# Performance work log

Hardware: AMD Instinct MI355X
Metric: run time of the kernel (lower is better)

The kernel has to match this reference:

```python
import jax, jax.numpy as jnp
import numpy as np
from jax import lax

CHUNK = 64
D_CONV = 4
EPS = 1e-5


def _rmsnorm(x, w):
    ms = jnp.mean(jnp.square(x.astype(jnp.float32)), axis=-1, keepdims=True)
    return x * lax.rsqrt(ms + EPS).astype(x.dtype) * w


def _conv_mix(x, proj_w, gate_w, conv_w, conv_b, out_proj_w):
    # x: [B,L,D] -> depthwise causal conv on projected channels, silu gate, out proj
    B, L, D = x.shape
    val = jnp.einsum('bld,ed->ble', x, proj_w)            # [B,L,d_inner]
    v = val.transpose(0, 2, 1)                            # [B,d_inner,L]
    d_inner = proj_w.shape[0]
    v = lax.conv_general_dilated(
        v, conv_w, window_strides=(1,), padding=[(D_CONV - 1, 0)],
        dimension_numbers=('NCH', 'OIH', 'NCH'), feature_group_count=d_inner)
    v = v + conv_b[None, :, None]
    val = jax.nn.silu(v.transpose(0, 2, 1))               # [B,L,d_inner]
    gate = jax.nn.silu(jnp.einsum('bld,ed->ble', x, gate_w))
    return jnp.einsum('ble,de->bld', val * gate, out_proj_w)


def _memory_attend(out, write_w, read_w, decay, log_alpha):
    B, T, D = out.shape
    C = CHUNK
    out32 = out.astype(jnp.float32)
    gamma = jax.nn.sigmoid(decay)
    log_gamma = jnp.log(gamma)
    v = jnp.einsum('btd,ed->bte', out32, write_w)         # proj_write
    wk = jnp.pad(out32[:, :-1], ((0, 0), (1, 0), (0, 0)))  # shifted keys
    rk = out32
    p = jnp.arange(C, dtype=jnp.float32)
    gp = gamma ** p                                       # [C]
    gw = gamma ** (C - 1 - p)                              # [C]
    diffs = jnp.maximum(p[:, None] - 1.0 - p[None, :], 0.0)
    M = jnp.exp(diffs * log_gamma) * (p[:, None] > p[None, :])  # [C,C]
    gC = gamma ** C
    Nc = T // C
    # scan axis first: [Nc,B,C,D]
    rk_c = rk.reshape(B, Nc, C, D).transpose(1, 0, 2, 3)
    wk_c = wk.reshape(B, Nc, C, D).transpose(1, 0, 2, 3)
    v_c = v.reshape(B, Nc, C, D).transpose(1, 0, 2, 3)

    def step(W, chunk):
        r, k, vv = chunk                                  # each [B,C,D]
        inter = jnp.einsum('bcd,bed->bce', r, W) * gp[None, :, None]
        S = jnp.einsum('bcd,bed->bce', r, k)              # [B,C,C]
        intra = jnp.einsum('bce,bed->bcd', S * M, vv)
        W_new = gC * W + jnp.einsum('bcd,bce->bde', vv * gw[None, :, None], k)
        return W_new, inter + intra

    W0 = jnp.zeros((B, D, D), dtype=jnp.float32)
    _, reads = lax.scan(step, W0, (rk_c, wk_c, v_c))      # [Nc,B,C,D]
    reads = reads.transpose(1, 0, 2, 3).reshape(B, T, D)
    read_out = jnp.einsum('btd,ed->bte', reads, read_w)
    return out + jnp.exp(log_alpha) * read_out.astype(out.dtype)


def setup_inputs() -> dict:
    key = jax.random.key(0)
    ks = jax.random.split(key, 9)
    B, T, D, d_inner = 8, 4096, 768, 1536
    s_d = 1.0 / np.sqrt(D)
    s_i = 1.0 / np.sqrt(d_inner)
    return {
        'x': jax.random.normal(ks[0], (B, T, D), jnp.float32),
        'norm_w': jnp.ones((D,), jnp.float32),
        'proj_w': jax.random.normal(ks[1], (d_inner, D), jnp.float32) * s_d,
        'gate_w': jax.random.normal(ks[2], (d_inner, D), jnp.float32) * s_d,
        'conv_w': jax.random.normal(ks[3], (d_inner, 1, D_CONV), jnp.float32) * 0.5,
        'conv_b': jnp.zeros((d_inner,), jnp.float32),
        'out_proj_w': jax.random.normal(ks[4], (D, d_inner), jnp.float32) * s_i,
        'write_w': jax.random.normal(ks[5], (D, D), jnp.float32) * s_d,
        'read_w': jax.random.normal(ks[6], (D, D), jnp.float32) * s_d,
        'decay': jnp.float32(4.6),
        'log_alpha': jnp.log(jnp.float32(0.03)),
    }


def reference(x, norm_w, proj_w, gate_w, conv_w, conv_b, out_proj_w, write_w, read_w, decay, log_alpha):
    out = _conv_mix(_rmsnorm(x, norm_w), proj_w, gate_w, conv_w, conv_b, out_proj_w)
    out = _memory_attend(out, write_w, read_w, decay, log_alpha)
    return x + out
```

## Files before the change

### kernel.cpp

```cpp
#include <hip/hip_runtime.h>
#include <stdint.h>


typedef short bf16s;
typedef __attribute__((ext_vector_type(8))) short short8;
typedef __attribute__((ext_vector_type(4))) float f32x4;

#define DEVINL __device__ __forceinline__

DEVINL float bf2f(short s) {
    union { unsigned u; float f; } v; v.u = ((unsigned)(unsigned short)s) << 16; return v.f;
}
DEVINL short f2bf(float f) {
    union { float f; unsigned u; } v; v.f = f;
    unsigned r = v.u + 0x7fffu + ((v.u >> 16) & 1u);
    return (short)(r >> 16);
}

DEVINL void glds16(void* lds, const void* g) {
    __builtin_amdgcn_global_load_lds(
        (const __attribute__((address_space(1))) void*)g,
        (__attribute__((address_space(3))) void*)lds, 16, 0, 0);
}

DEVINL void stage128(bf16s* lds, const bf16s* g, long gstride, int wave) {
#pragma unroll
    for (int p = 0; p < 4; ++p)
        glds16(lds + p * 2048 + wave * 512, g + (long)p * 32 * gstride);
}

DEVINL short8 fragr(const bf16s* t, int row, int kk, int q) {
    int f = kk * 4 + q;
    return *(const short8*)(t + row * 64 + ((f ^ (row & 7)) * 8));
}

#define MFMA(a, b, c) __builtin_amdgcn_mfma_f32_16x16x32_bf16((a), (b), (c), 0, 0, 0)

__global__ __launch_bounds__(256) void cast_w_kernel(
    const float* __restrict__ proj, const float* __restrict__ gate,
    const float* __restrict__ op, const float* __restrict__ wr, const float* __restrict__ rd,
    bf16s* __restrict__ w_pg, bf16s* __restrict__ w_op, bf16s* __restrict__ w_wr,
    bf16s* __restrict__ w_rd) {
    long i = (long)blockIdx.x * 256 + threadIdx.x;
    if (i < 1179648)        w_pg[i] = f2bf(proj[i]);
    else if (i < 2359296)   w_pg[i] = f2bf(gate[i - 1179648]);
    else if (i < 3538944)   w_op[i - 2359296] = f2bf(op[i - 2359296]);
    else if (i < 4128768)   w_wr[i - 3538944] = f2bf(wr[i - 3538944]);
    else if (i < 4718592)   w_rd[i - 4128768] = f2bf(rd[i - 4128768]);
}

__global__ __launch_bounds__(256) void rmsnorm_kernel(
    const float* __restrict__ x, const float* __restrict__ w, bf16s* __restrict__ xn) {
    long row = blockIdx.x;
    const float* xr = x + row * 768;
    int tid = threadIdx.x;
    float v0 = xr[tid], v1 = xr[tid + 256], v2 = xr[tid + 512];
    float ss = v0 * v0 + v1 * v1 + v2 * v2;
#pragma unroll
    for (int off = 32; off; off >>= 1) ss += __shfl_down(ss, off);
    __shared__ float p[4];
    if ((tid & 63) == 0) p[tid >> 6] = ss;
    __syncthreads();
    float tot = p[0] + p[1] + p[2] + p[3];
    float s = rsqrtf(tot * (1.0f / 768.0f) + 1e-5f);
    bf16s* o = xn + row * 768;
    o[tid]       = f2bf(v0 * s * w[tid]);
    o[tid + 256] = f2bf(v1 * s * w[tid + 256]);
    o[tid + 512] = f2bf(v2 * s * w[tid + 512]);
}

template <int MODE>
__global__ __launch_bounds__(256, 2) void gemm_kernel(
    const bf16s* __restrict__ A, const bf16s* __restrict__ B, int K, int N,
    bf16s* __restrict__ Cb, const float* __restrict__ xres,
    const bf16s* __restrict__ outres, const float* __restrict__ p_la,
    float* __restrict__ Cout) {
    __shared__ bf16s sA[128 * 64];
    __shared__ bf16s sB[128 * 64];
    const int tid = threadIdx.x;
    const int wave = tid >> 6, lane = tid & 63;
    const int wm = wave >> 1, wn = wave & 1;
    const int ln15 = lane & 15, q = lane >> 4;
    const long m0 = (long)blockIdx.y * 128, n0 = (long)blockIdx.x * 128;
    const int sr = tid >> 3;
    const int sf = (tid & 7) ^ (sr & 7);
    const bf16s* gA = A + (m0 + sr) * K + sf * 8;
    const bf16s* gB = B + (n0 + sr) * K + sf * 8;
    f32x4 acc[4][4] = {};
    const int nkt = K >> 6;
    for (int kt = 0; kt < nkt; ++kt) {
        __syncthreads();
        stage128(sA, gA, K, wave);
        stage128(sB, gB, K, wave);
        gA += 64; gB += 64;
        asm volatile("s_waitcnt vmcnt(0)" ::: "memory");
        __syncthreads();
#pragma unroll
        for (int kk = 0; kk < 2; ++kk) {
            short8 af[4], bf_[4];
#pragma unroll
            for (int i = 0; i < 4; ++i) af[i] = fragr(sA, wm * 64 + i * 16 + ln15, kk, q);
#pragma unroll
            for (int j = 0; j < 4; ++j) bf_[j] = fragr(sB, wn * 64 + j * 16 + ln15, kk, q);
#pragma unroll
            for (int i = 0; i < 4; ++i)
#pragma unroll
                for (int j = 0; j < 4; ++j) acc[i][j] = MFMA(af[i], bf_[j], acc[i][j]);
        }
    }
    float alpha = 0.f;
    if (MODE == 1) alpha = __expf(p_la[0]);
#pragma unroll
    for (int i = 0; i < 4; ++i)
#pragma unroll
        for (int j = 0; j < 4; ++j) {
            long mb = m0 + wm * 64 + i * 16 + q * 4;
            long nc = n0 + wn * 64 + j * 16 + ln15;
#pragma unroll
            for (int e = 0; e < 4; ++e) {
                long m = mb + e;
                float v = acc[i][j][e];
                if (MODE == 0) {
                    Cb[m * N + nc] = f2bf(v);
                } else {
                    long idx = m * 768 + nc;
                    Cout[idx] = xres[idx] + bf2f(outres[idx]) + alpha * v;
                }
            }
        }
}

__global__ __launch_bounds__(192) void conv_kernel(
    const bf16s* __restrict__ pg, const float* __restrict__ cw,
    const float* __restrict__ cb, bf16s* __restrict__ vg) {
    const int e0 = threadIdx.x * 8;
    const long l0 = (long)blockIdx.x * 16;
    float w0[8], w1[8], w2[8], w3[8], bias[8];
#pragma unroll
    for (int i = 0; i < 8; ++i) {
        const float* wc = cw + (e0 + i) * 4;
        w0[i] = wc[0]; w1[i] = wc[1]; w2[i] = wc[2]; w3[i] = wc[3];
        bias[i] = cb[e0 + i];
    }
    const bf16s* base = pg + l0 * 3072 + e0;
    short8 h0, h1, h2;
    if ((l0 & 4095) == 0) {
        short8 z = {0, 0, 0, 0, 0, 0, 0, 0};
        h0 = z; h1 = z; h2 = z;
    } else {
        h0 = *(const short8*)(base - 3 * 3072);
        h1 = *(const short8*)(base - 2 * 3072);
        h2 = *(const short8*)(base - 1 * 3072);
    }
    short8 cur = *(const short8*)base;
    short8 g8  = *(const short8*)(base + 1536);
    bf16s* out = vg + l0 * 1536 + e0;
#pragma unroll 4
    for (int t = 0; t < 16; ++t) {
        short8 ncur, ng;
        if (t < 15) {
            ncur = *(const short8*)(base + 3072);
            ng   = *(const short8*)(base + 3072 + 1536);
        }
        short8 o;
#pragma unroll
        for (int i = 0; i < 8; ++i) {
            float vv = bias[i] + bf2f(h0[i]) * w0[i] + bf2f(h1[i]) * w1[i]
                     + bf2f(h2[i]) * w2[i] + bf2f(cur[i]) * w3[i];
            float sv = vv / (1.0f + __expf(-vv));
            float gg = bf2f(g8[i]);
            o[i] = f2bf(sv * (gg / (1.0f + __expf(-gg))));
        }
        *(short8*)out = o;
        h0 = h1; h1 = h2; h2 = cur;
        cur = ncur; g8 = ng;
        base += 3072; out += 1536;
    }
}

template <int SHIFT, int GW>
__global__ __launch_bounds__(256) void transpose_kernel(
    const bf16s* __restrict__ src, bf16s* __restrict__ dst,
    const float* __restrict__ p_decay) {
    int b = blockIdx.z;
    long t0 = (long)blockIdx.y * 64, e0 = (long)blockIdx.x * 64;
    __shared__ bf16s tile[64][72];
    int tid = threadIdx.x;
    int r = tid >> 2, cs = (tid & 3) * 16;
    long tsrc = t0 + r - SHIFT;
    if (tsrc >= 0) {
        const bf16s* s = src + ((long)b * 4096 + tsrc) * 768 + e0 + cs;
        short8 v0 = *(const short8*)s;
        short8 v1 = *(const short8*)(s + 8);
        if (GW) {
            float gm = 1.0f / (1.0f + __expf(-p_decay[0]));
            float gwf = exp2f(__log2f(gm) * (float)(1023 - (int)(tsrc & 1023)));
#pragma unroll
            for (int i = 0; i < 8; ++i) {
                tile[r][cs + i]     = f2bf(bf2f(v0[i]) * gwf);
                tile[r][cs + 8 + i] = f2bf(bf2f(v1[i]) * gwf);
            }
        } else {
#pragma unroll
            for (int i = 0; i < 8; ++i) {
                tile[r][cs + i]     = v0[i];
                tile[r][cs + 8 + i] = v1[i];
            }
        }
    } else {
#pragma unroll
        for (int i = 0; i < 16; ++i) tile[r][cs + i] = 0;
    }
    __syncthreads();
    int er = tid >> 2, ts = (tid & 3) * 16;
    short8 a, bb;
#pragma unroll
    for (int i = 0; i < 8; ++i) a[i] = tile[ts + i][er];
#pragma unroll
    for (int i = 0; i < 8; ++i) bb[i] = tile[ts + 8 + i][er];
    bf16s* d = dst + ((long)b * 768 + e0 + er) * 4096 + t0 + ts;
    *(short8*)d = a;
    *(short8*)(d + 8) = bb;
}

__global__ __launch_bounds__(256, 2) void wstate_kernel(
    const bf16s* __restrict__ vTs, const bf16s* __restrict__ oTs,
    bf16s* __restrict__ Wst, const float* __restrict__ p_decay) {
    __shared__ bf16s sA[128 * 64];
    __shared__ bf16s sB[128 * 64];
    const int b = blockIdx.y;
    const int ti = blockIdx.x % 6, tj = blockIdx.x / 6;
    const int tid = threadIdx.x;
    const int wave = tid >> 6, lane = tid & 63;
    const int wm = wave >> 1, wn = wave & 1;
    const int ln15 = lane & 15, q = lane >> 4;
    const int sr = tid >> 3;
    const int sf = (tid & 7) ^ (sr & 7);
    const bf16s* gA = vTs + ((long)b * 768 + ti * 128 + sr) * 4096 + sf * 8;
    const bf16s* gB = oTs + ((long)b * 768 + tj * 128 + sr) * 4096 + sf * 8;
    const float gm = 1.0f / (1.0f + __expf(-p_decay[0]));
    const float gC = exp2f(__log2f(gm) * 1024.0f);
    f32x4 acc[4][4] = {};
    for (int jc = 0; jc < 4; ++jc) {
        bf16s* Wj = Wst + ((long)(b * 4 + jc)) * 768 * 768;
#pragma unroll
        for (int i = 0; i < 4; ++i)
#pragma unroll
            for (int jj = 0; jj < 4; ++jj) {
                long mb = ti * 128 + wm * 64 + i * 16 + q * 4;
                long nc = tj * 128 + wn * 64 + jj * 16 + ln15;
#pragma unroll
                for (int e = 0; e < 4; ++e) {
                    Wj[(mb + e) * 768 + nc] = f2bf(acc[i][jj][e]);
                    acc[i][jj][e] *= gC;
                }
            }
        for (int kt = 0; kt < 16; ++kt) {
            __syncthreads();
            stage128(sA, gA, 4096, wave);
            stage128(sB, gB, 4096, wave);
            gA += 64; gB += 64;
            asm volatile("s_waitcnt vmcnt(0)" ::: "memory");
            __syncthreads();
#pragma unroll
            for (int kk = 0; kk < 2; ++kk) {
                short8 af[4], bf_[4];
#pragma unroll
                for (int i = 0; i < 4; ++i) af[i] = fragr(sA, wm * 64 + i * 16 + ln15, kk, q);
#pragma unroll
                for (int j = 0; j < 4; ++j) bf_[j] = fragr(sB, wn * 64 + j * 16 + ln15, kk, q);
#pragma unroll
                for (int i = 0; i < 4; ++i)
#pragma unroll
                    for (int j = 0; j < 4; ++j) acc[i][j] = MFMA(af[i], bf_[j], acc[i][j]);
            }
        }
    }
}

__global__ __launch_bounds__(256, 2) void pmat_kernel(
    const bf16s* __restrict__ outb, bf16s* __restrict__ P,
    const float* __restrict__ p_decay) {
    const int ci = blockIdx.x >> 3, cj = blockIdx.x & 7;
    if (cj > ci) return;
    const int j = blockIdx.y, b = blockIdx.z;
    const bool fix = (j == 0 && cj == 0);
    __shared__ bf16s sA[128 * 64];
    __shared__ bf16s sB[128 * 64];
    const int tid = threadIdx.x;
    const int wave = tid >> 6, lane = tid & 63;
    const int wm = wave >> 1, wn = wave & 1;
    const int ln15 = lane & 15, q = lane >> 4;
    const int sr = tid >> 3;
    const int sf = (tid & 7) ^ (sr & 7);
    const bf16s* gA = outb + ((long)b * 4096 + j * 1024 + ci * 128 + sr) * 768 + sf * 8;
    const bf16s* gB = outb + ((long)b * 4096 + j * 1024 + cj * 128 + sr - 1) * 768 + sf * 8;
    f32x4 acc[4][4] = {};
    for (int kt = 0; kt < 12; ++kt) {
        __syncthreads();
        stage128(sA, gA, 768, wave);
        stage128(sB, gB, 768, wave);
        gA += 64; gB += 64;
        asm volatile("s_waitcnt vmcnt(0)" ::: "memory");
        __syncthreads();
        if (fix) {
            if (tid < 8) { short8 zz = {0,0,0,0,0,0,0,0}; ((short8*)sB)[tid] = zz; }
            __syncthreads();
        }
#pragma unroll
        for (int kk = 0; kk < 2; ++kk) {
            short8 af[4], bf_[4];
#pragma unroll
            for (int i = 0; i < 4; ++i) af[i] = fragr(sA, wm * 64 + i * 16 + ln15, kk, q);
#pragma unroll
            for (int jj = 0; jj < 4; ++jj) bf_[jj] = fragr(sB, wn * 64 + jj * 16 + ln15, kk, q);
#pragma unroll
            for (int i = 0; i < 4; ++i)
#pragma unroll
                for (int jj = 0; jj < 4; ++jj) acc[i][jj] = MFMA(af[i], bf_[jj], acc[i][jj]);
        }
    }
    const float lg = __log2f(1.0f / (1.0f + __expf(-p_decay[0])));
    bf16s* Pb = P + ((long)(b * 4 + j) << 20);
#pragma unroll
    for (int i = 0; i < 4; ++i)
#pragma unroll
        for (int jj = 0; jj < 4; ++jj) {
            int cb_ = ci * 128 + wm * 64 + i * 16 + q * 4;
            int cp  = cj * 128 + wn * 64 + jj * 16 + ln15;
#pragma unroll
            for (int e = 0; e < 4; ++e) {
                int c = cb_ + e;
                float val = (c > cp) ? acc[i][jj][e] * exp2f(lg * (float)(c - 1024)) : 0.0f;
                Pb[(long)c * 1024 + cp] = f2bf(val);
            }
        }
}

__global__ __launch_bounds__(256, 2) void reads_kernel(
    const bf16s* __restrict__ outb, const bf16s* __restrict__ Wst,
    const bf16s* __restrict__ Pm, const bf16s* __restrict__ vTs,
    bf16s* __restrict__ readsb, const float* __restrict__ p_decay) {
    const int ci = blockIdx.x & 7, vi = blockIdx.x >> 3;
    const int j = blockIdx.y, b = blockIdx.z;
    __shared__ bf16s sA[128 * 64];
    __shared__ bf16s sB[128 * 64];
    const int tid = threadIdx.x;
    const int wave = tid >> 6, lane = tid & 63;
    const int wm = wave >> 1, wn = wave & 1;
    const int ln15 = lane & 15, q = lane >> 4;
    const int sr = tid >> 3;
    const int sf = (tid & 7) ^ (sr & 7);
    const float lg = __log2f(1.0f / (1.0f + __expf(-p_decay[0])));
    f32x4 acc[4][4] = {};
    if (j > 0) {
        const bf16s* gA = outb + ((long)b * 4096 + j * 1024 + ci * 128 + sr) * 768 + sf * 8;
        const bf16s* gB = Wst + ((long)(b * 4 + j) * 768 + vi * 128 + sr) * 768 + sf * 8;
        for (int kt = 0; kt < 12; ++kt) {
            __syncthreads();
            stage128(sA, gA, 768, wave);
            stage128(sB, gB, 768, wave);
            gA += 64; gB += 64;
            asm volatile("s_waitcnt vmcnt(0)" ::: "memory");
            __syncthreads();
#pragma unroll
            for (int kk = 0; kk < 2; ++kk) {
                short8 af[4], bf_[4];
#pragma unroll
                for (int i = 0; i < 4; ++i) af[i] = fragr(sA, wm * 64 + i * 16 + ln15, kk, q);
#pragma unroll
                for (int jj = 0; jj < 4; ++jj) bf_[jj] = fragr(sB, wn * 64 + jj * 16 + ln15, kk, q);
#pragma unroll
                for (int i = 0; i < 4; ++i)
#pragma unroll
                    for (int jj = 0; jj < 4; ++jj) acc[i][jj] = MFMA(af[i], bf_[jj], acc[i][jj]);
            }
        }
#pragma unroll
        for (int i = 0; i < 4; ++i) {
            int cb_ = ci * 128 + wm * 64 + i * 16 + q * 4;
#pragma unroll
            for (int e = 0; e < 4; ++e) {
                float s = exp2f(lg * (float)(cb_ + e));
#pragma unroll
                for (int jj = 0; jj < 4; ++jj) acc[i][jj][e] *= s;
            }
        }
    }
    {
        const bf16s* gA = Pm + ((long)(b * 4 + j) << 20) + (long)(ci * 128 + sr) * 1024 + sf * 8;
        const bf16s* gB = vTs + ((long)b * 768 + vi * 128 + sr) * 4096 + j * 1024 + sf * 8;
        const int nkt = 2 * (ci + 1);
        for (int kt = 0; kt < nkt; ++kt) {
            __syncthreads();
            stage128(sA, gA, 1024, wave);
            stage128(sB, gB, 4096, wave);
            gA += 64; gB += 64;
            asm volatile("s_waitcnt vmcnt(0)" ::: "memory");
            __syncthreads();
#pragma unroll
            for (int kk = 0; kk < 2; ++kk) {
                short8 af[4], bf_[4];
#pragma unroll
                for (int i = 0; i < 4; ++i) af[i] = fragr(sA, wm * 64 + i * 16 + ln15, kk, q);
#pragma unroll
                for (int jj = 0; jj < 4; ++jj) bf_[jj] = fragr(sB, wn * 64 + jj * 16 + ln15, kk, q);
#pragma unroll
                for (int i = 0; i < 4; ++i)
#pragma unroll
                    for (int jj = 0; jj < 4; ++jj) acc[i][jj] = MFMA(af[i], bf_[jj], acc[i][jj]);
            }
        }
    }
#pragma unroll
    for (int i = 0; i < 4; ++i)
#pragma unroll
        for (int jj = 0; jj < 4; ++jj) {
            long tb = (long)j * 1024 + ci * 128 + wm * 64 + i * 16 + q * 4;
            long nc = vi * 128 + wn * 64 + jj * 16 + ln15;
#pragma unroll
            for (int e = 0; e < 4; ++e)
                readsb[((long)b * 4096 + tb + e) * 768 + nc] = f2bf(acc[i][jj][e]);
        }
}

extern "C" void kernel_launch(void* const* d_in, const int* in_sizes, int n_in,
                              void* d_out, int out_size, void* d_ws, size_t ws_size,
                              hipStream_t stream) {
    (void)in_sizes; (void)n_in; (void)out_size;
    const float* x      = (const float*)d_in[0];
    const float* norm_w = (const float*)d_in[1];
    const float* proj_w = (const float*)d_in[2];
    const float* gate_w = (const float*)d_in[3];
    const float* conv_w = (const float*)d_in[4];
    const float* conv_b = (const float*)d_in[5];
    const float* op_w   = (const float*)d_in[6];
    const float* wr_w   = (const float*)d_in[7];
    const float* rd_w   = (const float*)d_in[8];
    const float* decay  = (const float*)d_in[9];
    const float* la     = (const float*)d_in[10];

    char* ws = (char*)d_ws;
    size_t off = 0;
    auto alloc = [&](size_t bytes) { void* p = ws + off; off += (bytes + 255) & ~(size_t)255; return p; };
    bf16s* w_pg = (bf16s*)alloc(3072l * 768 * 2);
    bf16s* w_op = (bf16s*)alloc(768l * 1536 * 2);
    bf16s* w_wr = (bf16s*)alloc(768l * 768 * 2);
    bf16s* w_rd = (bf16s*)alloc(768l * 768 * 2);
    bf16s* RA   = (bf16s*)alloc(32768l * 768 * 2);
    bf16s* RB   = (bf16s*)alloc(2 * 32768l * 768 * 2);
    bf16s* RC   = (bf16s*)alloc(2 * 32768l * 768 * 2);
    bf16s* RE   = (bf16s*)alloc(32768l * 768 * 2);
    if (ws_size < off) return;

    bf16s* xn    = RA;
    bf16s* vTs   = RA;
    bf16s* pgH   = RB;
    bf16s* vb    = RB;
    bf16s* oTs   = RB + 25165824;
    bf16s* Pm    = RB;
    bf16s* vg    = RC;
    bf16s* Wst   = RC;
    bf16s* readsb= RC + 18874368;
    bf16s* outb  = RE;

    hipLaunchKernelGGL(cast_w_kernel, dim3(18432), dim3(256), 0, stream,
                       proj_w, gate_w, op_w, wr_w, rd_w, w_pg, w_op, w_wr, w_rd);
    hipLaunchKernelGGL(rmsnorm_kernel, dim3(32768), dim3(256), 0, stream, x, norm_w, xn);
    for (int h = 0; h < 2; ++h) {
        hipLaunchKernelGGL(HIP_KERNEL_NAME(gemm_kernel<0>), dim3(24, 128), dim3(256), 0, stream,
                           xn + (long)h * 16384 * 768, w_pg, 768, 3072, pgH,
                           (const float*)nullptr, (const bf16s*)nullptr, la, (float*)nullptr);
        hipLaunchKernelGGL(conv_kernel, dim3(1024), dim3(192), 0, stream,
                           pgH, conv_w, conv_b, vg + (long)h * 16384 * 1536);
    }
    hipLaunchKernelGGL(HIP_KERNEL_NAME(gemm_kernel<0>), dim3(6, 256), dim3(256), 0, stream,
                       vg, w_op, 1536, 768, outb,
                       (const float*)nullptr, (const bf16s*)nullptr, la, (float*)nullptr);
    hipLaunchKernelGGL(HIP_KERNEL_NAME(gemm_kernel<0>), dim3(6, 256), dim3(256), 0, stream,
                       outb, w_wr, 768, 768, vb,
                       (const float*)nullptr, (const bf16s*)nullptr, la, (float*)nullptr);
    hipLaunchKernelGGL(HIP_KERNEL_NAME(transpose_kernel<1, 0>), dim3(12, 64, 8), dim3(256), 0, stream,
                       outb, oTs, decay);
    hipLaunchKernelGGL(HIP_KERNEL_NAME(transpose_kernel<0, 1>), dim3(12, 64, 8), dim3(256), 0, stream,
                       vb, vTs, decay);
    hipLaunchKernelGGL(wstate_kernel, dim3(36, 8), dim3(256), 0, stream,
                       vTs, oTs, Wst, decay);
    hipLaunchKernelGGL(pmat_kernel, dim3(64, 4, 8), dim3(256), 0, stream,
                       outb, Pm, decay);
    hipLaunchKernelGGL(reads_kernel, dim3(48, 4, 8), dim3(256), 0, stream,
                       outb, Wst, Pm, vTs, readsb, decay);
    hipLaunchKernelGGL(HIP_KERNEL_NAME(gemm_kernel<1>), dim3(6, 256), dim3(256), 0, stream,
                       readsb, w_rd, 768, 768, (bf16s*)nullptr,
                       x, outb, la, (float*)d_out);
}
```

Baseline: 982.8 us.

## Replace GEMM with 256x256-tile 8-wave double-buffered pipelined kernel

Swaps the 128x128 single-buffered GEMM for a 256x256 tile kernel with 8 waves and double-buffered LDS. Global-to-LDS loads for the next k-slab are interleaved between MFMA quarters, using explicit barriers, partial vmcnt waits and setprio. This targets the load-then-compute serialization of the old loop and raises data reuse per tile. In exchange it uses 128KB LDS, more registers and fewer blocks, and the fine-grained manual sync adds correctness risk.

```diff
diff --git a/kernel.cpp b/kernel.cpp
--- a/kernel.cpp
+++ b/kernel.cpp
@@ -27,6 +27,12 @@
 #pragma unroll
     for (int p = 0; p < 4; ++p)
         glds16(lds + p * 2048 + wave * 512, g + (long)p * 32 * gstride);
+}
+
+DEVINL void stage_half512(bf16s* lds, const bf16s* g, long gstride, int wave) {
+#pragma unroll
+    for (int p = 0; p < 2; ++p)
+        glds16(lds + p * 4096 + wave * 512, g + (long)p * 64 * gstride);
 }
 
 DEVINL short8 fragr(const bf16s* t, int row, int kk, int q) {
@@ -69,61 +75,123 @@
     o[tid + 512] = f2bf(v2 * s * w[tid + 512]);
 }
 
+#define P_MID()                                                   \
+    asm volatile("" ::: "memory");                                \
+    __builtin_amdgcn_s_barrier();                                 \
+    asm volatile("s_waitcnt lgkmcnt(0)" ::: "memory");            \
+    __builtin_amdgcn_sched_barrier(0);                            \
+    __builtin_amdgcn_s_setprio(1)
+
+#define P_END()                                                   \
+    __builtin_amdgcn_s_setprio(0);                                \
+    asm volatile("" ::: "memory");                                \
+    __builtin_amdgcn_s_barrier();                                 \
+    asm volatile("" ::: "memory")
+
+#define P_END_VM()                                                \
+    __builtin_amdgcn_s_setprio(0);                                \
+    asm volatile("s_waitcnt vmcnt(4)" ::: "memory");              \
+    asm volatile("" ::: "memory");                                \
+    __builtin_amdgcn_s_barrier();                                 \
+    asm volatile("" ::: "memory")
+
+#define RD_A(dst, s, kk)                                          \
+    _Pragma("unroll")                                             \
+    for (int m = 0; m < 8; ++m) dst[m] = fragr(&sA[s][wm][0], m * 16 + ln15, kk, q)
+
+#define RD_B(dst, s, kk)                                          \
+    _Pragma("unroll")                                             \
+    for (int n = 0; n < 4; ++n) dst[n] = fragr(&sB[s][bh][0], (wn & 1) * 64 + n * 16 + ln15, kk, q)
+
+#define Q_MFMA(af, bfr, nlo)                                      \
+    _Pragma("unroll")                                             \
+    for (int m = 0; m < 8; ++m) {                                 \
+        acc[m][nlo]     = MFMA(af[m], bfr[nlo],     acc[m][nlo]);     \
+        acc[m][nlo + 1] = MFMA(af[m], bfr[nlo + 1], acc[m][nlo + 1]); \
+    }
+
 template <int MODE>
-__global__ __launch_bounds__(256, 2) void gemm_kernel(
+__global__ __launch_bounds__(512, 2) void gemm8_kernel(
     const bf16s* __restrict__ A, const bf16s* __restrict__ B, int K, int N,
     bf16s* __restrict__ Cb, const float* __restrict__ xres,
     const bf16s* __restrict__ outres, const float* __restrict__ p_la,
     float* __restrict__ Cout) {
-    __shared__ bf16s sA[128 * 64];
-    __shared__ bf16s sB[128 * 64];
+    __shared__ bf16s sA[2][2][8192];
+    __shared__ bf16s sB[2][2][8192];
     const int tid = threadIdx.x;
     const int wave = tid >> 6, lane = tid & 63;
-    const int wm = wave >> 1, wn = wave & 1;
+    const int wm = wave >> 2, wn = wave & 3;
+    const int bh = wn >> 1;
     const int ln15 = lane & 15, q = lane >> 4;
-    const long m0 = (long)blockIdx.y * 128, n0 = (long)blockIdx.x * 128;
+    const long m0 = (long)blockIdx.y * 256, n0 = (long)blockIdx.x * 256;
     const int sr = tid >> 3;
     const int sf = (tid & 7) ^ (sr & 7);
-    const bf16s* gA = A + (m0 + sr) * K + sf * 8;
-    const bf16s* gB = B + (n0 + sr) * K + sf * 8;
-    f32x4 acc[4][4] = {};
-    const int nkt = K >> 6;
-    for (int kt = 0; kt < nkt; ++kt) {
-        __syncthreads();
-        stage128(sA, gA, K, wave);
-        stage128(sB, gB, K, wave);
-        gA += 64; gB += 64;
-        asm volatile("s_waitcnt vmcnt(0)" ::: "memory");
-        __syncthreads();
-#pragma unroll
-        for (int kk = 0; kk < 2; ++kk) {
-            short8 af[4], bf_[4];
-#pragma unroll
-            for (int i = 0; i < 4; ++i) af[i] = fragr(sA, wm * 64 + i * 16 + ln15, kk, q);
-#pragma unroll
-            for (int j = 0; j < 4; ++j) bf_[j] = fragr(sB, wn * 64 + j * 16 + ln15, kk, q);
-#pragma unroll
-            for (int i = 0; i < 4; ++i)
-#pragma unroll
-                for (int j = 0; j < 4; ++j) acc[i][j] = MFMA(af[i], bf_[j], acc[i][j]);
-        }
-    }
+    const bf16s* pA0 = A + (m0 + sr) * K + sf * 8;
+    const bf16s* pA1 = A + (m0 + 128 + sr) * K + sf * 8;
+    const bf16s* pB0 = B + (n0 + sr) * K + sf * 8;
+    const bf16s* pB1 = B + (n0 + 128 + sr) * K + sf * 8;
+    const int NKT = K >> 6, NI = NKT >> 1;
+
+    stage_half512(&sA[0][0][0], pA0, K, wave);
+    stage_half512(&sA[0][1][0], pA1, K, wave);
+    stage_half512(&sB[0][0][0], pB0, K, wave);
+    stage_half512(&sB[0][1][0], pB1, K, wave);
+    stage_half512(&sA[1][0][0], pA0 + 64, K, wave);
+    stage_half512(&sA[1][1][0], pA1 + 64, K, wave);
+    asm volatile("s_waitcnt vmcnt(4)" ::: "memory");
+    asm volatile("" ::: "memory");
+    __builtin_amdgcn_s_barrier();
+    asm volatile("" ::: "memory");
+
+    f32x4 acc[8][4] = {};
+    short8 a0[8], a1[8], b0[4], b1[4];
+
+    for (int it = 0; it < NI; ++it) {
+        const long o1 = (long)(2 * it + 1) * 64;
+        int t2 = 2 * it + 2; if (t2 > NKT - 1) t2 = NKT - 1;
+        int t3 = 2 * it + 3; if (t3 > NKT - 1) t3 = NKT - 1;
+        const long o2 = (long)t2 * 64, o3 = (long)t3 * 64;
+        RD_A(a0, 0, 0); RD_B(b0, 0, 0);
+        stage_half512(&sB[1][0][0], pB0 + o1, K, wave);
+        P_MID(); Q_MFMA(a0, b0, 0); P_END();
+        RD_A(a1, 0, 1);
+        stage_half512(&sB[1][1][0], pB1 + o1, K, wave);
+        P_MID(); Q_MFMA(a0, b0, 2); P_END();
+        RD_B(b1, 0, 1);
+        stage_half512(&sA[0][0][0], pA0 + o2, K, wave);
+        P_MID(); Q_MFMA(a1, b1, 0); P_END();
+        stage_half512(&sA[0][1][0], pA1 + o2, K, wave);
+        P_MID(); Q_MFMA(a1, b1, 2); P_END_VM();
+        RD_A(a0, 1, 0); RD_B(b0, 1, 0);
+        stage_half512(&sB[0][0][0], pB0 + o2, K, wave);
+        P_MID(); Q_MFMA(a0, b0, 0); P_END();
+        RD_A(a1, 1, 1);
+        stage_half512(&sB[0][1][0], pB1 + o2, K, wave);
+        P_MID(); Q_MFMA(a0, b0, 2); P_END();
+        RD_B(b1, 1, 1);
+        stage_half512(&sA[1][0][0], pA0 + o3, K, wave);
+        P_MID(); Q_MFMA(a1, b1, 0); P_END();
+        stage_half512(&sA[1][1][0], pA1 + o3, K, wave);
+        P_MID(); Q_MFMA(a1, b1, 2); P_END_VM();
+    }
+    asm volatile("s_waitcnt vmcnt(0)" ::: "memory");
+
     float alpha = 0.f;
     if (MODE == 1) alpha = __expf(p_la[0]);
 #pragma unroll
-    for (int i = 0; i < 4; ++i)
-#pragma unroll
-        for (int j = 0; j < 4; ++j) {
-            long mb = m0 + wm * 64 + i * 16 + q * 4;
-            long nc = n0 + wn * 64 + j * 16 + ln15;
+    for (int m = 0; m < 8; ++m)
+#pragma unroll
+        for (int n = 0; n < 4; ++n) {
+            long mb = m0 + wm * 128 + m * 16 + q * 4;
+            long nc = n0 + wn * 64 + n * 16 + ln15;
 #pragma unroll
             for (int e = 0; e < 4; ++e) {
-                long m = mb + e;
-                float v = acc[i][j][e];
+                long mm = mb + e;
+                float v = acc[m][n][e];
                 if (MODE == 0) {
-                    Cb[m * N + nc] = f2bf(v);
+                    Cb[mm * N + nc] = f2bf(v);
                 } else {
-                    long idx = m * 768 + nc;
+                    long idx = mm * 768 + nc;
                     Cout[idx] = xres[idx] + bf2f(outres[idx]) + alpha * v;
                 }
             }
@@ -468,16 +536,16 @@
                        proj_w, gate_w, op_w, wr_w, rd_w, w_pg, w_op, w_wr, w_rd);
     hipLaunchKernelGGL(rmsnorm_kernel, dim3(32768), dim3(256), 0, stream, x, norm_w, xn);
     for (int h = 0; h < 2; ++h) {
-        hipLaunchKernelGGL(HIP_KERNEL_NAME(gemm_kernel<0>), dim3(24, 128), dim3(256), 0, stream,
+        hipLaunchKernelGGL(HIP_KERNEL_NAME(gemm8_kernel<0>), dim3(12, 64), dim3(512), 0, stream,
                            xn + (long)h * 16384 * 768, w_pg, 768, 3072, pgH,
                            (const float*)nullptr, (const bf16s*)nullptr, la, (float*)nullptr);
         hipLaunchKernelGGL(conv_kernel, dim3(1024), dim3(192), 0, stream,
                            pgH, conv_w, conv_b, vg + (long)h * 16384 * 1536);
     }
-    hipLaunchKernelGGL(HIP_KERNEL_NAME(gemm_kernel<0>), dim3(6, 256), dim3(256), 0, stream,
+    hipLaunchKernelGGL(HIP_KERNEL_NAME(gemm8_kernel<0>), dim3(3, 128), dim3(512), 0, stream,
                        vg, w_op, 1536, 768, outb,
                        (const float*)nullptr, (const bf16s*)nullptr, la, (float*)nullptr);
-    hipLaunchKernelGGL(HIP_KERNEL_NAME(gemm_kernel<0>), dim3(6, 256), dim3(256), 0, stream,
+    hipLaunchKernelGGL(HIP_KERNEL_NAME(gemm8_kernel<0>), dim3(3, 128), dim3(512), 0, stream,
                        outb, w_wr, 768, 768, vb,
                        (const float*)nullptr, (const bf16s*)nullptr, la, (float*)nullptr);
     hipLaunchKernelGGL(HIP_KERNEL_NAME(transpose_kernel<1, 0>), dim3(12, 64, 8), dim3(256), 0, stream,
@@ -490,7 +558,7 @@
                        outb, Pm, decay);
     hipLaunchKernelGGL(reads_kernel, dim3(48, 4, 8), dim3(256), 0, stream,
                        outb, Wst, Pm, vTs, readsb, decay);
-    hipLaunchKernelGGL(HIP_KERNEL_NAME(gemm_kernel<1>), dim3(6, 256), dim3(256), 0, stream,
+    hipLaunchKernelGGL(HIP_KERNEL_NAME(gemm8_kernel<1>), dim3(3, 128), dim3(512), 0, stream,
                        readsb, w_rd, 768, 768, (bf16s*)nullptr,
                        x, outb, la, (float*)d_out);
 }
```

Measured after the change: 1.047 ms. 6.6% more time.
